# Kernel optimization log

Measured on AMD Instinct MI355X. Metric: run time of the kernel, lower is better.

Reference implementation:

```python
import jax, jax.numpy as jnp
import numpy as np

NUM_HEADS = 8
SCALE_BASE = 512.0
GN_EPS = 1e-5


def rotate_every_two(x):
    x1 = x[..., ::2]
    x2 = x[..., 1::2]
    return jnp.stack([-x2, x1], axis=-1).reshape(x.shape)


def xpos_apply(x, downscale):
    # x: [B, T, D]; XPOS rotary with length-dependent scale (offset=0)
    L, D = x.shape[1], x.shape[2]
    half = D // 2
    scale_vec = (jnp.arange(0, D, 2, dtype=jnp.float32) + 0.4 * D) / (1.4 * D)  # [half]
    pos = jnp.arange(L, dtype=jnp.float32)
    scale = scale_vec[None, :] ** (pos[:, None] / SCALE_BASE)  # [L, half]
    inv_freq = 1.0 / (10000.0 ** (jnp.arange(half, dtype=jnp.float32) / half))
    sinusoid = pos[:, None] * inv_freq[None, :]  # [L, half]
    sin, cos = jnp.sin(sinusoid), jnp.cos(sinusoid)
    if downscale:
        scale = 1.0 / scale
    sin_s = jnp.repeat(sin * scale, 2, axis=-1)  # duplicate_interleave -> [L, D]
    cos_s = jnp.repeat(cos * scale, 2, axis=-1)
    return x * cos_s + rotate_every_two(x) * sin_s


def decay_mask_fn(T, num_heads):
    # gamma per head; decay stored as log(gamma) so mask = gamma^(i-j) on lower triangle
    s, e = np.log(1.0 / 32.0), np.log(1.0 / 512.0)
    gamma = 1.0 - jnp.exp(jnp.linspace(s, e, num_heads).astype(jnp.float32))
    log_decay = jnp.log(gamma)  # [H], negative
    idx = jnp.arange(T)
    expo = (idx[:, None] - idx[None, :]).astype(jnp.float32)  # i - j
    tri = (idx[:, None] >= idx[None, :])
    expo_safe = jnp.where(tri, expo, 0.0)
    mask = jnp.exp(log_decay[:, None, None] * expo_safe) * tri  # [H, T, T]
    scale = jnp.sqrt(mask.sum(axis=-1, keepdims=True))  # [H, T, 1]
    return mask / scale


def setup_inputs() -> dict:
    key = jax.random.key(0)
    ks = jax.random.split(key, 4)
    B, T, E = 2, 2048, 1024
    V = 2 * E
    return {
        "hidden_states": jax.random.normal(ks[0], (B, T, E), dtype=jnp.float32),
        "w_qkv": jax.random.normal(ks[1], (E, 2 * E + V), dtype=jnp.float32) * 0.02,
        "b_qkv": jnp.zeros((2 * E + V,), dtype=jnp.float32),
        "w_g": jax.random.normal(ks[2], (E, V), dtype=jnp.float32) * 0.02,
        "b_g": jnp.zeros((V,), dtype=jnp.float32),
        "w_p": jax.random.normal(ks[3], (V, E), dtype=jnp.float32) * 0.02,
        "b_p": jnp.zeros((E,), dtype=jnp.float32),
    }


def reference(hidden_states, w_qkv, b_qkv, w_g, b_g, w_p, b_p):
    B, T, E = hidden_states.shape
    H = NUM_HEADS
    V = 2 * E
    dk, dv = E // H, V // H

    qkv = hidden_states @ w_qkv + b_qkv
    q, k, v = qkv[..., :E], qkv[..., E:2 * E], qkv[..., 2 * E:]
    q = xpos_apply(q, downscale=False)
    k = xpos_apply(k, downscale=True)

    # split heads -> [B, H, T, d]
    q = q.reshape(B, T, H, dk).transpose(0, 2, 1, 3)
    k = k.reshape(B, T, H, dk).transpose(0, 2, 1, 3)
    v = v.reshape(B, T, H, dv).transpose(0, 2, 1, 3)

    mask = decay_mask_fn(T, H)  # [H, T, T]

    # parallel retention
    retention = jnp.einsum("bhid,bhjd->bhij", q, k) * (dk ** -0.5)
    retention = retention * mask[None]  # [B, H, T, T]
    out = jnp.einsum("bhij,bhjv->bhiv", retention, v)

    # current_kv = sum_j mask[h, -1, j] * k_j (x) v_j
    curr_kv = jnp.einsum("hj,bhjk,bhjv->bhkv", mask[:, -1, :], k, v)

    retention_out = out.transpose(0, 2, 1, 3).reshape(B, T, V)

    # GroupNorm(num_groups=H, affine=False) over v_dim channels
    g = retention_out.reshape(B * T, H, dv)
    mu = g.mean(axis=-1, keepdims=True)
    var = ((g - mu) ** 2).mean(axis=-1, keepdims=True)
    normed = ((g - mu) / jnp.sqrt(var + GN_EPS)).reshape(B, T, V)

    gated = jax.nn.silu(hidden_states @ w_g + b_g) * normed
    proj = gated @ w_p + b_p
    return proj, curr_kv
```

## Files before the change

### kernel.cpp

```cpp
#include <hip/hip_runtime.h>
#include <math.h>

#define BT      4096
#define T_SEQ   2048
#define E_DIM   1024
#define V_DIM   2048
#define DK      128
#define DV      256
#define QKV_LD  4096

typedef unsigned short ushort_t;
typedef __attribute__((ext_vector_type(8)))  short bf16x8;
typedef __attribute__((ext_vector_type(4)))  unsigned short u16x4;
typedef __attribute__((ext_vector_type(16))) float f32x16;

__device__ __forceinline__ void decay_params(int h, float& ld, float& gamma) {
    const float s0 = -3.4657359027997265f;
    const float e0 = -6.2383246250395092f;
    float lin = s0 + (e0 - s0) * ((float)h * (1.0f / 7.0f));
    gamma = 1.0f - expf(lin);
    ld = logf(gamma);
}

__device__ __forceinline__ short f2bf(float f) {
    unsigned u = __float_as_uint(f);
    unsigned r = (u + 0x7fffu + ((u >> 16) & 1u)) >> 16;
    return (short)r;
}
__device__ __forceinline__ float bf2f(ushort_t u) {
    return __uint_as_float((unsigned)u << 16);
}

__device__ __forceinline__ void async_copy16(void* lds, const void* g) {
    __builtin_amdgcn_global_load_lds(
        (const __attribute__((address_space(1))) unsigned int*)g,
        (__attribute__((address_space(3))) unsigned int*)lds, 16, 0, 0);
}

__global__ __launch_bounds__(256)
void f32_to_bf16_kernel(const float* __restrict__ in, ushort_t* __restrict__ out)
{
    int i = (blockIdx.x * 256 + threadIdx.x) * 8;
    float4 a = *(const float4*)&in[i];
    float4 b = *(const float4*)&in[i + 4];
    bf16x8 o;
    o[0] = f2bf(a.x); o[1] = f2bf(a.y); o[2] = f2bf(a.z); o[3] = f2bf(a.w);
    o[4] = f2bf(b.x); o[5] = f2bf(b.y); o[6] = f2bf(b.z); o[7] = f2bf(b.w);
    *(bf16x8*)&out[i] = o;
}

__global__ __launch_bounds__(256)
void transpose_w_kernel(const float* __restrict__ W, ushort_t* __restrict__ Wt,
                        int K, int N)
{
    __shared__ float tile[32][33];
    const int k0 = blockIdx.y * 32, n0 = blockIdx.x * 32;
    const int t = threadIdx.x;
    const int r = t >> 3, c = (t & 7) * 4;
    float4 v = *(const float4*)&W[(size_t)(k0 + r) * N + n0 + c];
    tile[r][c] = v.x; tile[r][c + 1] = v.y; tile[r][c + 2] = v.z; tile[r][c + 3] = v.w;
    __syncthreads();
    u16x4 o;
    o[0] = (ushort_t)f2bf(tile[c][r]);
    o[1] = (ushort_t)f2bf(tile[c + 1][r]);
    o[2] = (ushort_t)f2bf(tile[c + 2][r]);
    o[3] = (ushort_t)f2bf(tile[c + 3][r]);
    *(u16x4*)&Wt[(size_t)(n0 + r) * K + k0 + c] = o;
}

template<int EPI>
__global__ __launch_bounds__(256)
void gemm_bf16(const ushort_t* __restrict__ A, int lda,
               const ushort_t* __restrict__ Bt, int ldb,
               const float* __restrict__ bias,
               void* __restrict__ Cv, int ldc,
               const void* __restrict__ extra, int lde,
               int nkt)
{
    __shared__ ushort_t As[3 * 128 * 32];
    __shared__ ushort_t Bs[3 * 128 * 32];

    const int tid = threadIdx.x;
    const int w  = tid >> 6, l = tid & 63;
    const int lc = l & 31, q = l >> 5;
    const int wr = w >> 1, wc = w & 1;
    const int m0 = blockIdx.y * 128, n0 = blockIdx.x * 128;

    const int r0 = tid >> 2,         kc0 = (tid & 3) ^ ((r0 >> 1) & 3);
    const int r1 = (256 + tid) >> 2, kc1 = (tid & 3) ^ ((r1 >> 1) & 3);
    const ushort_t* gA0 = A  + (size_t)(m0 + r0) * lda + kc0 * 8;
    const ushort_t* gA1 = A  + (size_t)(m0 + r1) * lda + kc1 * 8;
    const ushort_t* gB0 = Bt + (size_t)(n0 + r0) * ldb + kc0 * 8;
    const ushort_t* gB1 = Bt + (size_t)(n0 + r1) * ldb + kc1 * 8;
    const int s0 = w * 512;
    const int s1 = 2048 + w * 512;

    const int sl = (lc >> 1) & 3;
    int aoff[2][2], boff[2][2];
    #pragma unroll
    for (int mi = 0; mi < 2; ++mi)
        #pragma unroll
        for (int ks = 0; ks < 2; ++ks) {
            const int kc = ks * 2 + q;
            aoff[mi][ks] = ((wr * 64 + mi * 32 + lc) * 4 + (kc ^ sl)) * 8;
            boff[mi][ks] = ((wc * 64 + mi * 32 + lc) * 4 + (kc ^ sl)) * 8;
        }

    f32x16 acc[2][2];
    #pragma unroll
    for (int mi = 0; mi < 2; ++mi)
        #pragma unroll
        for (int ni = 0; ni < 2; ++ni)
            #pragma unroll
            for (int e = 0; e < 16; ++e) acc[mi][ni][e] = 0.0f;

    auto stage = [&](int bb) {
        async_copy16(&As[bb + s0], gA0); async_copy16(&As[bb + s1], gA1);
        async_copy16(&Bs[bb + s0], gB0); async_copy16(&Bs[bb + s1], gB1);
        gA0 += 32; gA1 += 32; gB0 += 32; gB1 += 32;
    };
    auto compute = [&](int cb) {
        bf16x8 a[2][2], b[2][2];
        #pragma unroll
        for (int mi = 0; mi < 2; ++mi)
            #pragma unroll
            for (int ks = 0; ks < 2; ++ks) {
                a[mi][ks] = *(const bf16x8*)&As[cb + aoff[mi][ks]];
                b[mi][ks] = *(const bf16x8*)&Bs[cb + boff[mi][ks]];
            }
        #pragma unroll
        for (int ks = 0; ks < 2; ++ks)
            #pragma unroll
            for (int mi = 0; mi < 2; ++mi)
                #pragma unroll
                for (int ni = 0; ni < 2; ++ni)
                    acc[mi][ni] = __builtin_amdgcn_mfma_f32_32x32x16_bf16(
                        a[mi][ks], b[ni][ks], acc[mi][ni], 0, 0, 0);
    };

    stage(0); stage(4096);
    int bs = 8192;
    int bc = 0;
    for (int kt = 0; kt < nkt - 2; ++kt) {
        asm volatile("s_waitcnt vmcnt(4)" ::: "memory");
        __builtin_amdgcn_s_barrier();
        stage(bs);
        compute(bc);
        bs = bc;
        bc = (bc == 8192) ? 0 : bc + 4096;
    }
    asm volatile("s_waitcnt vmcnt(4)" ::: "memory");
    __builtin_amdgcn_s_barrier();
    compute(bc);
    bc = (bc == 8192) ? 0 : bc + 4096;
    asm volatile("s_waitcnt vmcnt(0)" ::: "memory");
    __builtin_amdgcn_s_barrier();
    compute(bc);

    #pragma unroll
    for (int ni = 0; ni < 2; ++ni) {
        const int col = n0 + wc * 64 + ni * 32 + lc;
        const float bb = bias[col];
        #pragma unroll
        for (int mi = 0; mi < 2; ++mi) {
            #pragma unroll
            for (int r = 0; r < 16; ++r) {
                const int row = m0 + wr * 64 + mi * 32 + (r & 3) + 8 * (r >> 2) + 4 * q;
                float val = acc[mi][ni][r] + bb;
                if (EPI == 0) {
                    ((float*)Cv)[(size_t)row * ldc + col] = val;
                } else {
                    const float e = bf2f(((const ushort_t*)extra)[(size_t)row * lde + col]);
                    val = val / (1.0f + expf(-val)) * e;
                    ((ushort_t*)Cv)[(size_t)row * ldc + col] = (ushort_t)f2bf(val);
                }
            }
        }
    }
}

__global__ __launch_bounds__(256)
void gemm_tm64(const ushort_t* __restrict__ A, int lda,
               const ushort_t* __restrict__ Bt, int ldb,
               const float* __restrict__ bias,
               float* __restrict__ C, int ldc, int nkt)
{
    __shared__ ushort_t As[3 * 64 * 32];
    __shared__ ushort_t Bs[3 * 128 * 32];

    const int tid = threadIdx.x;
    const int w  = tid >> 6, l = tid & 63;
    const int lc = l & 31, q = l >> 5;
    const int wr = w >> 1, wc = w & 1;
    const int m0 = blockIdx.y * 64, n0 = blockIdx.x * 128;

    const int rA = tid >> 2,          kcA = (tid & 3) ^ ((rA >> 1) & 3);
    const int rB1 = (256 + tid) >> 2, kcB1 = (tid & 3) ^ ((rB1 >> 1) & 3);
    const ushort_t* gA  = A  + (size_t)(m0 + rA)  * lda + kcA  * 8;
    const ushort_t* gB0 = Bt + (size_t)(n0 + rA)  * ldb + kcA  * 8;
    const ushort_t* gB1 = Bt + (size_t)(n0 + rB1) * ldb + kcB1 * 8;
    const int sA  = w * 512;
    const int sB0 = w * 512;
    const int sB1 = 2048 + w * 512;

    const int sl = (lc >> 1) & 3;
    int aoff[2], boff[2][2];
    #pragma unroll
    for (int ks = 0; ks < 2; ++ks) {
        const int kc = ks * 2 + q;
        const int mrow = wr * 32 + lc;
        aoff[ks] = (mrow * 4 + (kc ^ sl)) * 8;
        #pragma unroll
        for (int ni = 0; ni < 2; ++ni) {
            const int nrow = wc * 64 + ni * 32 + lc;
            boff[ni][ks] = (nrow * 4 + (kc ^ sl)) * 8;
        }
    }

    f32x16 acc[2];
    #pragma unroll
    for (int ni = 0; ni < 2; ++ni)
        #pragma unroll
        for (int e = 0; e < 16; ++e) acc[ni][e] = 0.0f;

    auto stage = [&](int ab, int bb) {
        async_copy16(&As[ab + sA], gA);
        async_copy16(&Bs[bb + sB0], gB0); async_copy16(&Bs[bb + sB1], gB1);
        gA += 32; gB0 += 32; gB1 += 32;
    };
    auto compute = [&](int ab, int bb) {
        bf16x8 a[2], b[2][2];
        #pragma unroll
        for (int ks = 0; ks < 2; ++ks) {
            a[ks] = *(const bf16x8*)&As[ab + aoff[ks]];
            b[0][ks] = *(const bf16x8*)&Bs[bb + boff[0][ks]];
            b[1][ks] = *(const bf16x8*)&Bs[bb + boff[1][ks]];
        }
        #pragma unroll
        for (int ks = 0; ks < 2; ++ks)
            #pragma unroll
            for (int ni = 0; ni < 2; ++ni)
                acc[ni] = __builtin_amdgcn_mfma_f32_32x32x16_bf16(
                    a[ks], b[ni][ks], acc[ni], 0, 0, 0);
    };

    stage(0, 0); stage(2048, 4096);
    int as_ = 4096, bs_ = 8192;
    int ac_ = 0,    bc_ = 0;
    for (int kt = 0; kt < nkt - 2; ++kt) {
        asm volatile("s_waitcnt vmcnt(3)" ::: "memory");
        __builtin_amdgcn_s_barrier();
        stage(as_, bs_);
        compute(ac_, bc_);
        as_ = ac_; bs_ = bc_;
        ac_ = (ac_ == 4096) ? 0 : ac_ + 2048;
        bc_ = (bc_ == 8192) ? 0 : bc_ + 4096;
    }
    asm volatile("s_waitcnt vmcnt(3)" ::: "memory");
    __builtin_amdgcn_s_barrier();
    compute(ac_, bc_);
    ac_ = (ac_ == 4096) ? 0 : ac_ + 2048;
    bc_ = (bc_ == 8192) ? 0 : bc_ + 4096;
    asm volatile("s_waitcnt vmcnt(0)" ::: "memory");
    __builtin_amdgcn_s_barrier();
    compute(ac_, bc_);

    #pragma unroll
    for (int ni = 0; ni < 2; ++ni) {
        const int col = n0 + wc * 64 + ni * 32 + lc;
        const float bb = bias[col];
        #pragma unroll
        for (int r = 0; r < 16; ++r) {
            const int row = m0 + wr * 32 + (r & 3) + 8 * (r >> 2) + 4 * q;
            C[(size_t)row * ldc + col] = acc[ni][r] + bb;
        }
    }
}

__global__ __launch_bounds__(256)
void qk_prep(const float* __restrict__ qkv,
             ushort_t* __restrict__ qh, ushort_t* __restrict__ kh)
{
    const int row = blockIdx.x;
    const int t = threadIdx.x;
    const int b = row >> 11, trow = row & (T_SEQ - 1);
    const bool isK = t >= 128;
    const int col0 = (t & 127) * 8;
    const int h = col0 >> 7, d = col0 & 127;

    float ld, gamma;
    decay_params(h, ld, gamma);
    const float gsc = __expf(isK ? -ld * (float)(trow & 63) : ld * (float)(trow & 63));

    const float* src = qkv + (size_t)row * QKV_LD + (isK ? E_DIM : 0) + col0;
    float4 x0 = *(const float4*)src;
    float4 x1 = *(const float4*)(src + 4);
    float xv[8] = {x0.x, x0.y, x0.z, x0.w, x1.x, x1.y, x1.z, x1.w};

    const float tf = (float)trow * (1.0f / 512.0f);
    bf16x8 o;
    #pragma unroll
    for (int pi = 0; pi < 4; ++pi) {
        const int ip = col0 / 2 + pi;
        float sv = (2.0f * (float)ip + 409.6f) * (1.0f / 1433.6f);
        float e = __logf(sv) * tf;
        if (isK) e = -e;
        float sc = __expf(e);
        float invf = __expf((float)ip * -0.017988946038999563f);
        float sn, cs;
        sincosf((float)trow * invf, &sn, &cs);
        float c = cs * sc * gsc, s = sn * sc * gsc;
        float a = xv[2 * pi], bb = xv[2 * pi + 1];
        o[2 * pi]     = f2bf(a * c - bb * s);
        o[2 * pi + 1] = f2bf(bb * c + a * s);
    }
    ushort_t* dst = (isK ? kh : qh) + ((size_t)(b * 8 + h) * T_SEQ + trow) * 128 + d;
    *(bf16x8*)dst = o;
}

__global__ __launch_bounds__(256)
void v_transpose(const float* __restrict__ qkv, ushort_t* __restrict__ vt)
{
    __shared__ float tile[32][33];
    const int j0 = blockIdx.x * 32;
    const int zz = blockIdx.y;
    const int bh = zz >> 3, v0 = (zz & 7) * 32;
    const int b = bh >> 3, h = bh & 7;
    const int t = threadIdx.x;
    const int r = t >> 3, c = (t & 7) * 4;

    float4 x = *(const float4*)(qkv + (size_t)(b * T_SEQ + j0 + r) * QKV_LD
                                + 2 * E_DIM + h * DV + v0 + c);
    tile[r][c] = x.x; tile[r][c+1] = x.y; tile[r][c+2] = x.z; tile[r][c+3] = x.w;
    __syncthreads();
    u16x4 o;
    o[0] = (ushort_t)f2bf(tile[c][r]);
    o[1] = (ushort_t)f2bf(tile[c + 1][r]);
    o[2] = (ushort_t)f2bf(tile[c + 2][r]);
    o[3] = (ushort_t)f2bf(tile[c + 3][r]);
    *(u16x4*)&vt[((size_t)bh * 256 + v0 + r) * T_SEQ + j0 + c] = o;
}

__global__ __launch_bounds__(256)
void kt2_kernel(const ushort_t* __restrict__ kh, ushort_t* __restrict__ kt2)
{
    __shared__ ushort_t tile[32][40];
    const int j0 = blockIdx.x * 32;
    const int zz = blockIdx.y;
    const int bh = zz >> 2, k0 = (zz & 3) * 32;
    const int t = threadIdx.x;
    const int r = t >> 3, c = (t & 7) * 4;
    float ld, gamma; decay_params(bh & 7, ld, gamma);
    const float g63 = expf(ld * 63.0f);
    *(u16x4*)&tile[r][c] = *(const u16x4*)&kh[((size_t)bh * T_SEQ + j0 + r) * 128 + k0 + c];
    __syncthreads();
    u16x4 o;
    o[0] = (ushort_t)f2bf(bf2f(tile[c][r])     * g63);
    o[1] = (ushort_t)f2bf(bf2f(tile[c + 1][r]) * g63);
    o[2] = (ushort_t)f2bf(bf2f(tile[c + 2][r]) * g63);
    o[3] = (ushort_t)f2bf(bf2f(tile[c + 3][r]) * g63);
    *(u16x4*)&kt2[((size_t)bh * 128 + k0 + r) * T_SEQ + j0 + c] = o;
}

__global__ __launch_bounds__(256)
void chunk_kv(const ushort_t* __restrict__ vt, const ushort_t* __restrict__ kt2,
              ushort_t* __restrict__ Abuf)
{
    const int c = blockIdx.x;
    const int bh = blockIdx.y;
    const int tid = threadIdx.x;
    const int w = tid >> 6, l = tid & 63, lc = l & 31, q = l >> 5;
    const int j0 = c * 64;

    f32x16 acc[2][4];
    #pragma unroll
    for (int mi = 0; mi < 2; ++mi)
        #pragma unroll
        for (int ni = 0; ni < 4; ++ni)
            #pragma unroll
            for (int e = 0; e < 16; ++e) acc[mi][ni][e] = 0.0f;

    #pragma unroll
    for (int ks = 0; ks < 4; ++ks) {
        bf16x8 a[2], bfr[4];
        #pragma unroll
        for (int mi = 0; mi < 2; ++mi)
            a[mi] = *(const bf16x8*)(vt + ((size_t)bh * 256 + w * 64 + mi * 32 + lc) * T_SEQ
                                     + j0 + ks * 16 + q * 8);
        #pragma unroll
        for (int ni = 0; ni < 4; ++ni)
            bfr[ni] = *(const bf16x8*)(kt2 + ((size_t)bh * 128 + ni * 32 + lc) * T_SEQ
                                       + j0 + ks * 16 + q * 8);
        #pragma unroll
        for (int mi = 0; mi < 2; ++mi)
            #pragma unroll
            for (int ni = 0; ni < 4; ++ni)
                acc[mi][ni] = __builtin_amdgcn_mfma_f32_32x32x16_bf16(
                    a[mi], bfr[ni], acc[mi][ni], 0, 0, 0);
    }

    ushort_t* ab = Abuf + (size_t)(bh * 32 + c) * 256 * 128;
    #pragma unroll
    for (int mi = 0; mi < 2; ++mi)
        #pragma unroll
        for (int ni = 0; ni < 4; ++ni)
            #pragma unroll
            for (int r = 0; r < 16; ++r) {
                const int v = w * 64 + mi * 32 + (r & 3) + 8 * (r >> 2) + 4 * q;
                const int k = ni * 32 + lc;
                ab[(size_t)v * 128 + k] = (ushort_t)f2bf(acc[mi][ni][r]);
            }
}

__global__ __launch_bounds__(256)
void scan_state(const ushort_t* __restrict__ Abuf, ushort_t* __restrict__ St,
                float* __restrict__ ckv)
{
    const int blk = blockIdx.x;
    const int bh = blk >> 7, sub = blk & 127;
    const int tid = threadIdx.x;
    const int v = sub * 2 + (tid >> 7), k = tid & 127;

    float ld, gamma;
    decay_params(bh & 7, ld, gamma);
    const float g64 = expf(ld * 64.0f);

    const size_t base = ((size_t)bh * 32 * 256 + v) * 128 + k;
    const size_t cstr = 256 * 128;
    float s = 0.0f;
    for (int c = 0; c < 32; ++c) {
        const size_t off = base + (size_t)c * cstr;
        St[off] = (ushort_t)f2bf(gamma * s);
        s = g64 * s + bf2f(Abuf[off]);
    }
    const float inv_scale = rsqrtf((1.0f - expf(ld * (float)T_SEQ)) / (1.0f - gamma));
    ckv[((size_t)bh * 128 + k) * 256 + v] = s * inv_scale;
}

__global__ __launch_bounds__(64)
void retention_chunk(const ushort_t* __restrict__ qh,
                     const ushort_t* __restrict__ kh,
                     const ushort_t* __restrict__ vt,
                     const ushort_t* __restrict__ St,
                     ushort_t* __restrict__ normed)
{
    const int it = blockIdx.x;
    const int bh = blockIdx.y;
    const int b = bh >> 3, h = bh & 7;
    const int c = it >> 1, w = it & 1;
    const int l = threadIdx.x, lc = l & 31, q = l >> 5;
    const int i0 = it * 32;
    const size_t bhT = (size_t)bh * T_SEQ;

    float ld, gamma;
    decay_params(h, ld, gamma);

    bf16x8 qf[8];
    {
        const ushort_t* qp = qh + (bhT + i0 + lc) * 128 + q * 8;
        #pragma unroll
        for (int c8 = 0; c8 < 8; ++c8)
            qf[c8] = *(const bf16x8*)(qp + c8 * 16);
    }

    f32x16 acc[8];
    #pragma unroll
    for (int vg = 0; vg < 8; ++vg)
        #pragma unroll
        for (int e = 0; e < 16; ++e) acc[vg][e] = 0.0f;

    if (c > 0) {
        const ushort_t* sp = St + ((size_t)(bh * 32 + c) * 256 + lc) * 128 + q * 8;
        #pragma unroll
        for (int vg = 0; vg < 8; ++vg) {
            const ushort_t* spv = sp + (size_t)vg * 32 * 128;
            #pragma unroll
            for (int ks = 0; ks < 8; ++ks) {
                bf16x8 sb = *(const bf16x8*)(spv + ks * 16);
                acc[vg] = __builtin_amdgcn_mfma_f32_32x32x16_bf16(
                    qf[ks], sb, acc[vg], 0, 0, 0);
            }
        }
    }

    for (int jt2 = 0; jt2 <= w; ++jt2) {
        const int j0 = c * 64 + jt2 * 32;

        f32x16 s;
        #pragma unroll
        for (int e = 0; e < 16; ++e) s[e] = 0.0f;
        const ushort_t* kp = kh + (bhT + j0 + lc) * 128 + q * 8;
        #pragma unroll
        for (int c8 = 0; c8 < 8; ++c8) {
            bf16x8 ka = *(const bf16x8*)(kp + c8 * 16);
            s = __builtin_amdgcn_mfma_f32_32x32x16_bf16(ka, qf[c8], s, 0, 0, 0);
        }

        float sv[16];
        #pragma unroll
        for (int r = 0; r < 16; ++r) {
            float val = s[r];
            if (jt2 == w) {
                int jr_ = (r & 3) + 8 * (r >> 2) + 4 * q;
                val = (jr_ <= lc) ? val : 0.0f;
            }
            sv[r] = val;
        }

        bf16x8 pa0, pa1;
        #pragma unroll
        for (int e = 0; e < 4; ++e) {
            float t1 = __shfl_xor(sv[e + 4], 32);
            float t0 = __shfl_xor(sv[e], 32);
            pa0[e]     = f2bf(q ? t1 : sv[e]);
            pa0[e + 4] = f2bf(q ? sv[e + 4] : t0);
            float t3 = __shfl_xor(sv[e + 12], 32);
            float t2 = __shfl_xor(sv[e + 8], 32);
            pa1[e]     = f2bf(q ? t3 : sv[e + 8]);
            pa1[e + 4] = f2bf(q ? sv[e + 12] : t2);
        }

        #pragma unroll
        for (int vg = 0; vg < 8; ++vg) {
            const ushort_t* vp = vt + ((size_t)bh * 256 + vg * 32 + lc) * T_SEQ + j0 + q * 8;
            bf16x8 vb0 = *(const bf16x8*)vp;
            bf16x8 vb1 = *(const bf16x8*)(vp + 16);
            acc[vg] = __builtin_amdgcn_mfma_f32_32x32x16_bf16(pa0, vb0, acc[vg], 0, 0, 0);
            acc[vg] = __builtin_amdgcn_mfma_f32_32x32x16_bf16(pa1, vb1, acc[vg], 0, 0, 0);
        }
    }

    #pragma unroll
    for (int r = 0; r < 16; ++r) {
        const int il = (r & 3) + 8 * (r >> 2) + 4 * q;
        const int i  = i0 + il;
        float denom = (1.0f - expf(ld * (float)(i + 1))) / (1.0f - gamma);
        float fs = 0.08838834764831845f * rsqrtf(denom);
        float vals[8];
        float a1 = 0.0f, a2 = 0.0f;
        #pragma unroll
        for (int vg = 0; vg < 8; ++vg) {
            float x = acc[vg][r] * fs;
            vals[vg] = x;
            a1 += x; a2 += x * x;
        }
        a1 += __shfl_xor(a1, 1);  a2 += __shfl_xor(a2, 1);
        a1 += __shfl_xor(a1, 2);  a2 += __shfl_xor(a2, 2);
        a1 += __shfl_xor(a1, 4);  a2 += __shfl_xor(a2, 4);
        a1 += __shfl_xor(a1, 8);  a2 += __shfl_xor(a2, 8);
        a1 += __shfl_xor(a1, 16); a2 += __shfl_xor(a2, 16);
        float mu = a1 * (1.0f / 256.0f);
        float var = a2 * (1.0f / 256.0f) - mu * mu;
        float rs = rsqrtf(var + 1e-5f);
        ushort_t* op = normed + ((size_t)(b * T_SEQ + i)) * V_DIM + h * DV + lc;
        #pragma unroll
        for (int vg = 0; vg < 8; ++vg)
            op[vg * 32] = (ushort_t)f2bf((vals[vg] - mu) * rs);
    }
}

extern "C" void kernel_launch(void* const* d_in, const int* in_sizes, int n_in,
                              void* d_out, int out_size, void* d_ws, size_t ws_size,
                              hipStream_t stream)
{
    const float* hs    = (const float*)d_in[0];
    const float* w_qkv = (const float*)d_in[1];
    const float* b_qkv = (const float*)d_in[2];
    const float* w_g   = (const float*)d_in[3];
    const float* b_g   = (const float*)d_in[4];
    const float* w_p   = (const float*)d_in[5];
    const float* b_p   = (const float*)d_in[6];
    float* out = (float*)d_out;

    const size_t MB = 1024 * 1024;
    float*    qkv      = (float*)d_ws;
    ushort_t* Abuf     = (ushort_t*)d_ws;
    ushort_t* normed   = (ushort_t*)d_ws;
    ushort_t* Stbuf    = (ushort_t*)((char*)d_ws + 32 * MB);
    ushort_t* gated_bf = (ushort_t*)((char*)d_ws + 32 * MB);
    ushort_t* wg_t     = (ushort_t*)((char*)d_ws + 56 * MB);
    ushort_t* wp_t     = (ushort_t*)((char*)d_ws + 60 * MB);
    ushort_t* qh       = (ushort_t*)((char*)d_ws + 64 * MB);
    ushort_t* vt       = (ushort_t*)((char*)d_ws + 72 * MB);
    ushort_t* wqkv_t   = (ushort_t*)((char*)d_ws + 88 * MB);
    ushort_t* kh       = (ushort_t*)((char*)d_ws + 88 * MB);
    ushort_t* hs_bf    = (ushort_t*)d_out;
    ushort_t* kt2      = (ushort_t*)((char*)d_out + 8 * MB);
    float*    ckv_out  = out + (size_t)BT * E_DIM;

    f32_to_bf16_kernel<<<dim3(2048), 256, 0, stream>>>(hs, hs_bf);
    transpose_w_kernel<<<dim3(128, 32), 256, 0, stream>>>(w_qkv, wqkv_t, E_DIM, 4096);

    gemm_bf16<0><<<dim3(32, 32), 256, 0, stream>>>(
        hs_bf, E_DIM, wqkv_t, E_DIM, b_qkv, qkv, QKV_LD, nullptr, 0, E_DIM / 32);

    qk_prep<<<dim3(BT), 256, 0, stream>>>(qkv, qh, kh);
    v_transpose<<<dim3(64, 128), 256, 0, stream>>>(qkv, vt);
    kt2_kernel<<<dim3(64, 64), 256, 0, stream>>>(kh, kt2);

    chunk_kv<<<dim3(32, 16), 256, 0, stream>>>(vt, kt2, Abuf);
    scan_state<<<dim3(2048), 256, 0, stream>>>(Abuf, Stbuf, ckv_out);
    retention_chunk<<<dim3(64, 16), 64, 0, stream>>>(qh, kh, vt, Stbuf, normed);

    transpose_w_kernel<<<dim3(64, 32), 256, 0, stream>>>(w_g, wg_t, E_DIM, V_DIM);
    transpose_w_kernel<<<dim3(32, 64), 256, 0, stream>>>(w_p, wp_t, V_DIM, E_DIM);

    gemm_bf16<1><<<dim3(16, 32), 256, 0, stream>>>(
        hs_bf, E_DIM, wg_t, E_DIM, b_g, gated_bf, V_DIM, normed, V_DIM, E_DIM / 32);

    gemm_tm64<<<dim3(8, 64), 256, 0, stream>>>(
        gated_bf, V_DIM, wp_t, V_DIM, b_p, out, E_DIM, V_DIM / 32);
}
```

Measured before the change: 307.7 us.

## Replace QKV GEMM with 256x256-tile, 8-wave ping-pong pipelined bf16 kernel

Adds a new GEMM for the QKV projection that uses 256x256 output tiles, 512 threads, a K-step of 64, and double-buffered LDS. Global loads are interleaved with MFMA phases, using s_setprio and explicit waitcnt/barrier scheduling. The larger tiles are meant to raise data reuse and hide memory latency better than the 128x128 kernel. The grid shrinks to 256 blocks, which may underfill the CUs, and the hand-written waitcnt ordering is fragile.

```diff
diff --git a/kernel.cpp b/kernel.cpp
--- a/kernel.cpp
+++ b/kernel.cpp
@@ -68,6 +68,254 @@
     *(u16x4*)&Wt[(size_t)(n0 + r) * K + k0 + c] = o;
 }
 
+__global__ __launch_bounds__(512, 2)
+void gemm256p8(const ushort_t* __restrict__ A,
+               const ushort_t* __restrict__ Bt,
+               const float* __restrict__ bias,
+               float* __restrict__ C, int ldc, int nkt)
+{
+    __shared__ ushort_t As[2 * 16384];
+    __shared__ ushort_t Bs[2 * 16384];
+
+    const int tid = threadIdx.x;
+    const int wid = tid >> 6, l = tid & 63;
+    const int lc = l & 31, q = l >> 5;
+    const int wr = wid >> 2, wc = wid & 3;
+    const int m0 = blockIdx.y * 256, n0 = blockIdx.x * 256;
+
+    const int sra = tid >> 3;
+    const int spa = (tid & 7) ^ (sra & 7);
+    const ushort_t* gA = A + (size_t)(m0 + sra) * 1024 + spa * 8;
+    const int srb = tid >> 2;
+    const int spb = (tid & 3) ^ ((srb >> 1) & 3);
+    const ushort_t* gB = Bt + (size_t)(n0 + srb) * 1024 + spb * 8;
+    const int da = tid * 8;
+
+    int arow0 = (wr * 128 +  0 + lc) * 64;
+    int arow1 = (wr * 128 + 32 + lc) * 64;
+    int arow2 = (wr * 128 + 64 + lc) * 64;
+    int arow3 = (wr * 128 + 96 + lc) * 64;
+    int sk0 = ((0 * 2 + q) ^ (lc & 7)) * 8;
+    int sk1 = ((1 * 2 + q) ^ (lc & 7)) * 8;
+    int sk2 = ((2 * 2 + q) ^ (lc & 7)) * 8;
+    int sk3 = ((3 * 2 + q) ^ (lc & 7)) * 8;
+    int brow0 = (wc * 64 +  0 + lc) * 32;
+    int brow1 = (wc * 64 + 32 + lc) * 32;
+    int tk0 = ((0 + q) ^ ((lc >> 1) & 3)) * 8;
+    int tk1 = ((2 + q) ^ ((lc >> 1) & 3)) * 8;
+    int tk2 = 8192 + ((0 + q) ^ ((lc >> 1) & 3)) * 8;
+    int tk3 = 8192 + ((2 + q) ^ ((lc >> 1) & 3)) * 8;
+
+    f32x16 acc[4][2];
+    #pragma unroll
+    for (int mi = 0; mi < 4; ++mi)
+        #pragma unroll
+        for (int ni = 0; ni < 2; ++ni)
+            #pragma unroll
+            for (int e = 0; e < 16; ++e) acc[mi][ni][e] = 0.0f;
+
+    async_copy16(&As[da],          gA);
+    async_copy16(&As[8192 + da],   gA + 131072);
+    async_copy16(&Bs[da],          gB);
+    async_copy16(&Bs[4096 + da],   gB + 131072);
+    async_copy16(&As[4096 + da],   gA + 65536);
+    async_copy16(&As[12288 + da],  gA + 196608);
+    async_copy16(&Bs[8192 + da],   gB + 32);
+    async_copy16(&Bs[12288 + da],  gB + 131072 + 32);
+    gA += 64; gB += 64;
+    asm volatile("s_waitcnt vmcnt(0)" ::: "memory");
+    __builtin_amdgcn_s_barrier();
+
+    int cur = 0;
+    for (int t = 0; t < nkt - 1; ++t) {
+        const int cb = cur * 16384;
+        const int nb = 16384 - cb;
+        bf16x8 a00 = *(const bf16x8*)&As[cb + arow0 + sk0];
+        bf16x8 a01 = *(const bf16x8*)&As[cb + arow0 + sk1];
+        bf16x8 a10 = *(const bf16x8*)&As[cb + arow1 + sk0];
+        bf16x8 a11 = *(const bf16x8*)&As[cb + arow1 + sk1];
+        bf16x8 b00 = *(const bf16x8*)&Bs[cb + brow0 + tk0];
+        bf16x8 b01 = *(const bf16x8*)&Bs[cb + brow0 + tk1];
+        bf16x8 b10 = *(const bf16x8*)&Bs[cb + brow1 + tk0];
+        bf16x8 b11 = *(const bf16x8*)&Bs[cb + brow1 + tk1];
+        async_copy16(&As[nb + da],        gA);
+        async_copy16(&As[nb + 8192 + da], gA + 131072);
+        async_copy16(&Bs[nb + da],        gB);
+        async_copy16(&Bs[nb + 4096 + da], gB + 131072);
+        __builtin_amdgcn_s_barrier();
+        asm volatile("s_waitcnt lgkmcnt(0)" ::: "memory");
+        __builtin_amdgcn_s_setprio(1);
+        acc[0][0] = __builtin_amdgcn_mfma_f32_32x32x16_bf16(a00, b00, acc[0][0], 0, 0, 0);
+        acc[0][1] = __builtin_amdgcn_mfma_f32_32x32x16_bf16(a00, b10, acc[0][1], 0, 0, 0);
+        acc[1][0] = __builtin_amdgcn_mfma_f32_32x32x16_bf16(a10, b00, acc[1][0], 0, 0, 0);
+        acc[1][1] = __builtin_amdgcn_mfma_f32_32x32x16_bf16(a10, b10, acc[1][1], 0, 0, 0);
+        acc[0][0] = __builtin_amdgcn_mfma_f32_32x32x16_bf16(a01, b01, acc[0][0], 0, 0, 0);
+        acc[0][1] = __builtin_amdgcn_mfma_f32_32x32x16_bf16(a01, b11, acc[0][1], 0, 0, 0);
+        acc[1][0] = __builtin_amdgcn_mfma_f32_32x32x16_bf16(a11, b01, acc[1][0], 0, 0, 0);
+        acc[1][1] = __builtin_amdgcn_mfma_f32_32x32x16_bf16(a11, b11, acc[1][1], 0, 0, 0);
+        __builtin_amdgcn_s_setprio(0);
+        asm volatile("s_waitcnt vmcnt(6)" ::: "memory");
+        __builtin_amdgcn_s_barrier();
+        bf16x8 a20 = *(const bf16x8*)&As[cb + arow2 + sk0];
+        bf16x8 a21 = *(const bf16x8*)&As[cb + arow2 + sk1];
+        bf16x8 a30 = *(const bf16x8*)&As[cb + arow3 + sk0];
+        bf16x8 a31 = *(const bf16x8*)&As[cb + arow3 + sk1];
+        async_copy16(&As[nb + 4096 + da],  gA + 65536);
+        async_copy16(&As[nb + 12288 + da], gA + 196608);
+        __builtin_amdgcn_s_barrier();
+        asm volatile("s_waitcnt lgkmcnt(0)" ::: "memory");
+        __builtin_amdgcn_s_setprio(1);
+        acc[2][0] = __builtin_amdgcn_mfma_f32_32x32x16_bf16(a20, b00, acc[2][0], 0, 0, 0);
+        acc[2][1] = __builtin_amdgcn_mfma_f32_32x32x16_bf16(a20, b10, acc[2][1], 0, 0, 0);
+        acc[3][0] = __builtin_amdgcn_mfma_f32_32x32x16_bf16(a30, b00, acc[3][0], 0, 0, 0);
+        acc[3][1] = __builtin_amdgcn_mfma_f32_32x32x16_bf16(a30, b10, acc[3][1], 0, 0, 0);
+        acc[2][0] = __builtin_amdgcn_mfma_f32_32x32x16_bf16(a21, b01, acc[2][0], 0, 0, 0);
+        acc[2][1] = __builtin_amdgcn_mfma_f32_32x32x16_bf16(a21, b11, acc[2][1], 0, 0, 0);
+        acc[3][0] = __builtin_amdgcn_mfma_f32_32x32x16_bf16(a31, b01, acc[3][0], 0, 0, 0);
+        acc[3][1] = __builtin_amdgcn_mfma_f32_32x32x16_bf16(a31, b11, acc[3][1], 0, 0, 0);
+        __builtin_amdgcn_s_setprio(0);
+        asm volatile("s_waitcnt vmcnt(6)" ::: "memory");
+        __builtin_amdgcn_s_barrier();
+        bf16x8 a02 = *(const bf16x8*)&As[cb + arow0 + sk2];
+        bf16x8 a03 = *(const bf16x8*)&As[cb + arow0 + sk3];
+        bf16x8 a12 = *(const bf16x8*)&As[cb + arow1 + sk2];
+        bf16x8 a13 = *(const bf16x8*)&As[cb + arow1 + sk3];
+        bf16x8 b02 = *(const bf16x8*)&Bs[cb + brow0 + tk2];
+        bf16x8 b03 = *(const bf16x8*)&Bs[cb + brow0 + tk3];
+        bf16x8 b12 = *(const bf16x8*)&Bs[cb + brow1 + tk2];
+        bf16x8 b13 = *(const bf16x8*)&Bs[cb + brow1 + tk3];
+        async_copy16(&Bs[nb + 8192 + da],  gB + 32);
+        async_copy16(&Bs[nb + 12288 + da], gB + 131072 + 32);
+        gA += 64; gB += 64;
+        __builtin_amdgcn_s_barrier();
+        asm volatile("s_waitcnt lgkmcnt(0)" ::: "memory");
+        __builtin_amdgcn_s_setprio(1);
+        acc[0][0] = __builtin_amdgcn_mfma_f32_32x32x16_bf16(a02, b02, acc[0][0], 0, 0, 0);
+        acc[0][1] = __builtin_amdgcn_mfma_f32_32x32x16_bf16(a02, b12, acc[0][1], 0, 0, 0);
+        acc[1][0] = __builtin_amdgcn_mfma_f32_32x32x16_bf16(a12, b02, acc[1][0], 0, 0, 0);
+        acc[1][1] = __builtin_amdgcn_mfma_f32_32x32x16_bf16(a12, b12, acc[1][1], 0, 0, 0);
+        acc[0][0] = __builtin_amdgcn_mfma_f32_32x32x16_bf16(a03, b03, acc[0][0], 0, 0, 0);
+        acc[0][1] = __builtin_amdgcn_mfma_f32_32x32x16_bf16(a03, b13, acc[0][1], 0, 0, 0);
+        acc[1][0] = __builtin_amdgcn_mfma_f32_32x32x16_bf16(a13, b03, acc[1][0], 0, 0, 0);
+        acc[1][1] = __builtin_amdgcn_mfma_f32_32x32x16_bf16(a13, b13, acc[1][1], 0, 0, 0);
+        __builtin_amdgcn_s_setprio(0);
+        __builtin_amdgcn_s_barrier();
+        bf16x8 a22 = *(const bf16x8*)&As[cb + arow2 + sk2];
+        bf16x8 a23 = *(const bf16x8*)&As[cb + arow2 + sk3];
+        bf16x8 a32 = *(const bf16x8*)&As[cb + arow3 + sk2];
+        bf16x8 a33 = *(const bf16x8*)&As[cb + arow3 + sk3];
+        __builtin_amdgcn_s_barrier();
+        asm volatile("s_waitcnt lgkmcnt(0)" ::: "memory");
+        __builtin_amdgcn_s_setprio(1);
+        acc[2][0] = __builtin_amdgcn_mfma_f32_32x32x16_bf16(a22, b02, acc[2][0], 0, 0, 0);
+        acc[2][1] = __builtin_amdgcn_mfma_f32_32x32x16_bf16(a22, b12, acc[2][1], 0, 0, 0);
+        acc[3][0] = __builtin_amdgcn_mfma_f32_32x32x16_bf16(a32, b02, acc[3][0], 0, 0, 0);
+        acc[3][1] = __builtin_amdgcn_mfma_f32_32x32x16_bf16(a32, b12, acc[3][1], 0, 0, 0);
+        acc[2][0] = __builtin_amdgcn_mfma_f32_32x32x16_bf16(a23, b03, acc[2][0], 0, 0, 0);
+        acc[2][1] = __builtin_amdgcn_mfma_f32_32x32x16_bf16(a23, b13, acc[2][1], 0, 0, 0);
+        acc[3][0] = __builtin_amdgcn_mfma_f32_32x32x16_bf16(a33, b03, acc[3][0], 0, 0, 0);
+        acc[3][1] = __builtin_amdgcn_mfma_f32_32x32x16_bf16(a33, b13, acc[3][1], 0, 0, 0);
+        __builtin_amdgcn_s_setprio(0);
+        asm volatile("s_waitcnt vmcnt(4)" ::: "memory");
+        __builtin_amdgcn_s_barrier();
+        cur ^= 1;
+    }
+
+    {
+        const int cb = cur * 16384;
+        bf16x8 a00 = *(const bf16x8*)&As[cb + arow0 + sk0];
+        bf16x8 a01 = *(const bf16x8*)&As[cb + arow0 + sk1];
+        bf16x8 a10 = *(const bf16x8*)&As[cb + arow1 + sk0];
+        bf16x8 a11 = *(const bf16x8*)&As[cb + arow1 + sk1];
+        bf16x8 b00 = *(const bf16x8*)&Bs[cb + brow0 + tk0];
+        bf16x8 b01 = *(const bf16x8*)&Bs[cb + brow0 + tk1];
+        bf16x8 b10 = *(const bf16x8*)&Bs[cb + brow1 + tk0];
+        bf16x8 b11 = *(const bf16x8*)&Bs[cb + brow1 + tk1];
+        __builtin_amdgcn_s_barrier();
+        asm volatile("s_waitcnt lgkmcnt(0)" ::: "memory");
+        __builtin_amdgcn_s_setprio(1);
+        acc[0][0] = __builtin_amdgcn_mfma_f32_32x32x16_bf16(a00, b00, acc[0][0], 0, 0, 0);
+        acc[0][1] = __builtin_amdgcn_mfma_f32_32x32x16_bf16(a00, b10, acc[0][1], 0, 0, 0);
+        acc[1][0] = __builtin_amdgcn_mfma_f32_32x32x16_bf16(a10, b00, acc[1][0], 0, 0, 0);
+        acc[1][1] = __builtin_amdgcn_mfma_f32_32x32x16_bf16(a10, b10, acc[1][1], 0, 0, 0);
+        acc[0][0] = __builtin_amdgcn_mfma_f32_32x32x16_bf16(a01, b01, acc[0][0], 0, 0, 0);
+        acc[0][1] = __builtin_amdgcn_mfma_f32_32x32x16_bf16(a01, b11, acc[0][1], 0, 0, 0);
+        acc[1][0] = __builtin_amdgcn_mfma_f32_32x32x16_bf16(a11, b01, acc[1][0], 0, 0, 0);
+        acc[1][1] = __builtin_amdgcn_mfma_f32_32x32x16_bf16(a11, b11, acc[1][1], 0, 0, 0);
+        __builtin_amdgcn_s_setprio(0);
+        asm volatile("s_waitcnt vmcnt(2)" ::: "memory");
+        __builtin_amdgcn_s_barrier();
+        bf16x8 a20 = *(const bf16x8*)&As[cb + arow2 + sk0];
+        bf16x8 a21 = *(const bf16x8*)&As[cb + arow2 + sk1];
+        bf16x8 a30 = *(const bf16x8*)&As[cb + arow3 + sk0];
+        bf16x8 a31 = *(const bf16x8*)&As[cb + arow3 + sk1];
+        __builtin_amdgcn_s_barrier();
+        asm volatile("s_waitcnt lgkmcnt(0)" ::: "memory");
+        __builtin_amdgcn_s_setprio(1);
+        acc[2][0] = __builtin_amdgcn_mfma_f32_32x32x16_bf16(a20, b00, acc[2][0], 0, 0, 0);
+        acc[2][1] = __builtin_amdgcn_mfma_f32_32x32x16_bf16(a20, b10, acc[2][1], 0, 0, 0);
+        acc[3][0] = __builtin_amdgcn_mfma_f32_32x32x16_bf16(a30, b00, acc[3][0], 0, 0, 0);
+        acc[3][1] = __builtin_amdgcn_mfma_f32_32x32x16_bf16(a30, b10, acc[3][1], 0, 0, 0);
+        acc[2][0] = __builtin_amdgcn_mfma_f32_32x32x16_bf16(a21, b01, acc[2][0], 0, 0, 0);
+        acc[2][1] = __builtin_amdgcn_mfma_f32_32x32x16_bf16(a21, b11, acc[2][1], 0, 0, 0);
+        acc[3][0] = __builtin_amdgcn_mfma_f32_32x32x16_bf16(a31, b01, acc[3][0], 0, 0, 0);
+        acc[3][1] = __builtin_amdgcn_mfma_f32_32x32x16_bf16(a31, b11, acc[3][1], 0, 0, 0);
+        __builtin_amdgcn_s_setprio(0);
+        asm volatile("s_waitcnt vmcnt(0)" ::: "memory");
+        __builtin_amdgcn_s_barrier();
+        bf16x8 a02 = *(const bf16x8*)&As[cb + arow0 + sk2];
+        bf16x8 a03 = *(const bf16x8*)&As[cb + arow0 + sk3];
+        bf16x8 a12 = *(const bf16x8*)&As[cb + arow1 + sk2];
+        bf16x8 a13 = *(const bf16x8*)&As[cb + arow1 + sk3];
+        bf16x8 b02 = *(const bf16x8*)&Bs[cb + brow0 + tk2];
+        bf16x8 b03 = *(const bf16x8*)&Bs[cb + brow0 + tk3];
+        bf16x8 b12 = *(const bf16x8*)&Bs[cb + brow1 + tk2];
+        bf16x8 b13 = *(const bf16x8*)&Bs[cb + brow1 + tk3];
+        __builtin_amdgcn_s_barrier();
+        asm volatile("s_waitcnt lgkmcnt(0)" ::: "memory");
+        __builtin_amdgcn_s_setprio(1);
+        acc[0][0] = __builtin_amdgcn_mfma_f32_32x32x16_bf16(a02, b02, acc[0][0], 0, 0, 0);
+        acc[0][1] = __builtin_amdgcn_mfma_f32_32x32x16_bf16(a02, b12, acc[0][1], 0, 0, 0);
+        acc[1][0] = __builtin_amdgcn_mfma_f32_32x32x16_bf16(a12, b02, acc[1][0], 0, 0, 0);
+        acc[1][1] = __builtin_amdgcn_mfma_f32_32x32x16_bf16(a12, b12, acc[1][1], 0, 0, 0);
+        acc[0][0] = __builtin_amdgcn_mfma_f32_32x32x16_bf16(a03, b03, acc[0][0], 0, 0, 0);
+        acc[0][1] = __builtin_amdgcn_mfma_f32_32x32x16_bf16(a03, b13, acc[0][1], 0, 0, 0);
+        acc[1][0] = __builtin_amdgcn_mfma_f32_32x32x16_bf16(a13, b03, acc[1][0], 0, 0, 0);
+        acc[1][1] = __builtin_amdgcn_mfma_f32_32x32x16_bf16(a13, b13, acc[1][1], 0, 0, 0);
+        __builtin_amdgcn_s_setprio(0);
+        __builtin_amdgcn_s_barrier();
+        bf16x8 a22 = *(const bf16x8*)&As[cb + arow2 + sk2];
+        bf16x8 a23 = *(const bf16x8*)&As[cb + arow2 + sk3];
+        bf16x8 a32 = *(const bf16x8*)&As[cb + arow3 + sk2];
+        bf16x8 a33 = *(const bf16x8*)&As[cb + arow3 + sk3];
+        asm volatile("s_waitcnt lgkmcnt(0)" ::: "memory");
+        __builtin_amdgcn_s_setprio(1);
+        acc[2][0] = __builtin_amdgcn_mfma_f32_32x32x16_bf16(a22, b02, acc[2][0], 0, 0, 0);
+        acc[2][1] = __builtin_amdgcn_mfma_f32_32x32x16_bf16(a22, b12, acc[2][1], 0, 0, 0);
+        acc[3][0] = __builtin_amdgcn_mfma_f32_32x32x16_bf16(a32, b02, acc[3][0], 0, 0, 0);
+        acc[3][1] = __builtin_amdgcn_mfma_f32_32x32x16_bf16(a32, b12, acc[3][1], 0, 0, 0);
+        acc[2][0] = __builtin_amdgcn_mfma_f32_32x32x16_bf16(a23, b03, acc[2][0], 0, 0, 0);
+        acc[2][1] = __builtin_amdgcn_mfma_f32_32x32x16_bf16(a23, b13, acc[2][1], 0, 0, 0);
+        acc[3][0] = __builtin_amdgcn_mfma_f32_32x32x16_bf16(a33, b03, acc[3][0], 0, 0, 0);
+        acc[3][1] = __builtin_amdgcn_mfma_f32_32x32x16_bf16(a33, b13, acc[3][1], 0, 0, 0);
+        __builtin_amdgcn_s_setprio(0);
+    }
+
+    #pragma unroll
+    for (int ni = 0; ni < 2; ++ni) {
+        const int col = n0 + wc * 64 + ni * 32 + lc;
+        const float bb = bias[col];
+        #pragma unroll
+        for (int mi = 0; mi < 4; ++mi) {
+            #pragma unroll
+            for (int r = 0; r < 16; ++r) {
+                const int row = m0 + wr * 128 + mi * 32 + (r & 3) + 8 * (r >> 2) + 4 * q;
+                C[(size_t)row * ldc + col] = acc[mi][ni][r] + bb;
+            }
+        }
+    }
+}
+
 template<int EPI>
 __global__ __launch_bounds__(256)
 void gemm_bf16(const ushort_t* __restrict__ A, int lda,
@@ -101,9 +349,9 @@
     for (int mi = 0; mi < 2; ++mi)
         #pragma unroll
         for (int ks = 0; ks < 2; ++ks) {
-            const int kc = ks * 2 + q;
-            aoff[mi][ks] = ((wr * 64 + mi * 32 + lc) * 4 + (kc ^ sl)) * 8;
-            boff[mi][ks] = ((wc * 64 + mi * 32 + lc) * 4 + (kc ^ sl)) * 8;
+            const int kk = ks * 2 + q;
+            aoff[mi][ks] = ((wr * 64 + mi * 32 + lc) * 4 + (kk ^ sl)) * 8;
+            boff[mi][ks] = ((wc * 64 + mi * 32 + lc) * 4 + (kk ^ sl)) * 8;
         }
 
     f32x16 acc[2][2];
@@ -207,13 +455,13 @@
     int aoff[2], boff[2][2];
     #pragma unroll
     for (int ks = 0; ks < 2; ++ks) {
-        const int kc = ks * 2 + q;
+        const int kk = ks * 2 + q;
         const int mrow = wr * 32 + lc;
-        aoff[ks] = (mrow * 4 + (kc ^ sl)) * 8;
+        aoff[ks] = (mrow * 4 + (kk ^ sl)) * 8;
         #pragma unroll
         for (int ni = 0; ni < 2; ++ni) {
             const int nrow = wc * 64 + ni * 32 + lc;
-            boff[ni][ks] = (nrow * 4 + (kc ^ sl)) * 8;
+            boff[ni][ks] = (nrow * 4 + (kk ^ sl)) * 8;
         }
     }
 
@@ -591,8 +839,8 @@
     f32_to_bf16_kernel<<<dim3(2048), 256, 0, stream>>>(hs, hs_bf);
     transpose_w_kernel<<<dim3(128, 32), 256, 0, stream>>>(w_qkv, wqkv_t, E_DIM, 4096);
 
-    gemm_bf16<0><<<dim3(32, 32), 256, 0, stream>>>(
-        hs_bf, E_DIM, wqkv_t, E_DIM, b_qkv, qkv, QKV_LD, nullptr, 0, E_DIM / 32);
+    gemm256p8<<<dim3(16, 16), 512, 0, stream>>>(
+        hs_bf, wqkv_t, b_qkv, qkv, QKV_LD, E_DIM / 64);
 
     qk_prep<<<dim3(BT), 256, 0, stream>>>(qkv, qh, kh);
     v_transpose<<<dim3(64, 128), 256, 0, stream>>>(qkv, vt);
```

New measurement: 303.2 us. Within noise of the previous version (-1.5%).
